# Kernel optimization log

Measured on AMD Instinct MI355X. Metric: run time of the kernel, lower is better.

Reference implementation:

```python
import jax, jax.numpy as jnp
import numpy as np

N_NODES = 50000


def _degrees(idx, n):
    d = jax.ops.segment_sum(jnp.ones(idx.shape, jnp.float32), idx, num_segments=n)
    return jnp.clip(d, 1.0)  # DGL clamps degree at 1


def gcn_layer(x, src, dst, W, b, n):
    """DGL GraphConv with norm='both': D_dst^-1/2 * sum_edges(D_src^-1/2 * x_src) @ W + b.
    Applies W before aggregation when in_feats > out_feats (cheaper), matching DGL."""
    inv_sqrt_out = _degrees(src, n) ** -0.5  # out-degree norm on source side
    inv_sqrt_in = _degrees(dst, n) ** -0.5   # in-degree norm on dest side
    h = x * inv_sqrt_out[:, None]
    if W.shape[0] > W.shape[1]:
        h = h @ W
        agg = jax.ops.segment_sum(h[src], dst, num_segments=n)
    else:
        agg = jax.ops.segment_sum(h[src], dst, num_segments=n)
        agg = agg @ W
    return agg * inv_sqrt_in[:, None] + b


def setup_inputs() -> dict:
    key = jax.random.key(0)
    ks = jax.random.split(key, 8)
    E = 800000
    in_feat = jax.random.normal(ks[0], (N_NODES, 1), dtype=jnp.float32)
    edge_index = jax.random.randint(ks[1], (2, E), 0, N_NODES, dtype=jnp.int32)
    def glorot(k, fan_in, fan_out):
        s = (6.0 / (fan_in + fan_out)) ** 0.5
        return jax.random.uniform(k, (fan_in, fan_out), jnp.float32, -s, s)
    W0 = glorot(ks[2], 1, 100); b0 = jnp.zeros((100,), jnp.float32)
    W1 = glorot(ks[3], 100, 10); b1 = jnp.zeros((10,), jnp.float32)
    W2 = glorot(ks[4], 10, 1); b2 = jnp.zeros((1,), jnp.float32)
    return {"in_feat": in_feat, "edge_index": edge_index,
            "W0": W0, "b0": b0, "W1": W1, "b1": b1, "W2": W2, "b2": b2}


def reference(in_feat, edge_index, W0, b0, W1, b1, W2, b2):
    src, dst = edge_index[0], edge_index[1]
    n = N_NODES
    h = gcn_layer(in_feat, src, dst, W0, b0, n)
    h = jax.nn.leaky_relu(h, negative_slope=0.01)
    h = gcn_layer(h, src, dst, W1, b1, n)
    h = jax.nn.relu(h)
    h = gcn_layer(h, src, dst, W2, b2, n)
    h = jax.nn.relu(h)
    return h
```

## Files before the change

### kernel.cpp

```cpp
#include <hip/hip_runtime.h>


#define NT 256
#define NTB 1024
#define K_BKT 250
#define R_NODES 200
#define SEG 48
#define CAP 4096
#define CHUNK 4096
#define BIN_BLOCKS 196
#define NSLOT (BIN_BLOCKS * SEG)
#define FINF 3.0e38f


__global__ __launch_bounds__(NT) void k_bin(const int4* __restrict__ src4,
                                            const int4* __restrict__ dst4, int E4,
                                            unsigned short* __restrict__ cntd16,
                                            unsigned short* __restrict__ cnts16,
                                            unsigned* __restrict__ dstSeg,
                                            unsigned short* __restrict__ srcSeg) {
  __shared__ unsigned cnt_d[K_BKT], cnt_s[K_BKT];
  int t = threadIdx.x, blk = blockIdx.x;
  for (int k = t; k < K_BKT; k += NT) { cnt_d[k] = 0u; cnt_s[k] = 0u; }
  __syncthreads();
  int base4 = blk * (CHUNK / 4);
  int4 sA[4], dA[4];
#pragma unroll
  for (int j = 0; j < 4; j++) {
    int e4 = base4 + j * NT + t;
    if (e4 < E4) { sA[j] = src4[e4]; dA[j] = dst4[e4]; }
    else { sA[j] = make_int4(-1, -1, -1, -1); dA[j] = make_int4(-1, -1, -1, -1); }
  }
  const int* sp = (const int*)sA;
  const int* dp = (const int*)dA;
#pragma unroll
  for (int j = 0; j < 16; j++) {
    int d = dp[j], s = sp[j];
    if (d >= 0) {
      unsigned bd = (unsigned)d / R_NODES;
      unsigned pd = atomicAdd(&cnt_d[bd], 1u);
      if (pd < SEG)
        dstSeg[((size_t)bd * BIN_BLOCKS + blk) * SEG + pd] =
            (unsigned)s | (((unsigned)d - bd * R_NODES) << 16);
      unsigned bs = (unsigned)s / R_NODES;
      unsigned ps = atomicAdd(&cnt_s[bs], 1u);
      if (ps < SEG)
        srcSeg[((size_t)bs * BIN_BLOCKS + blk) * SEG + ps] =
            (unsigned short)((unsigned)s - bs * R_NODES);
    }
  }
  __syncthreads();
  for (int k = t; k < K_BKT; k += NT) {
    unsigned cd = cnt_d[k]; if (cd > SEG) cd = SEG;
    unsigned cs = cnt_s[k]; if (cs > SEG) cs = SEG;
    cntd16[(size_t)blk * K_BKT + k] = (unsigned short)cd;
    cnts16[(size_t)blk * K_BKT + k] = (unsigned short)cs;
  }
}


struct BktLds {
  unsigned dslab[NSLOT];
  unsigned short sslab[NSLOT];
  unsigned cnt[R_NODES], cnts[R_NODES], cur[R_NODES];
  unsigned sc[256];
  unsigned short crow_d[256], crow_s[256];
  unsigned short stage[CAP];
};
struct PreLds {
  float W0s[100], b0s[100], W1s[1000];
  float beta[100], bsorted[128];
  int ord[100];
  float cA[1000], cB[1000];
  float baseA[16], baseB[16];
};
union BPool { BktLds b; PreLds p; };

__global__ __launch_bounds__(NTB) void k_bucket(
    const unsigned short* __restrict__ cntd16, const unsigned short* __restrict__ cnts16,
    const unsigned* __restrict__ dstSeg, const unsigned short* __restrict__ srcSeg,
    const float* __restrict__ x,
    const float* __restrict__ W0, const float* __restrict__ b0,
    const float* __restrict__ W1,
    float* __restrict__ betas, float* __restrict__ Aseg, float* __restrict__ Bseg,
    unsigned short* __restrict__ csr16,
    unsigned* __restrict__ rs, unsigned* __restrict__ rd,
    float* __restrict__ dsrc_inv, float* __restrict__ ddst_inv,
    float* __restrict__ s0, int n, int nbin) {
  __shared__ BPool u;
  int t = threadIdx.x, blk = blockIdx.x;
  if (blk < K_BKT) {
    const int b = blk;
    const int4* dsl4 = (const int4*)(dstSeg + (size_t)b * NSLOT);
    int4* dl4 = (int4*)u.b.dslab;
    for (int i = t; i < NSLOT / 4; i += NTB) dl4[i] = dsl4[i];
    const int4* ssl4 = (const int4*)(srcSeg + (size_t)b * NSLOT);
    int4* sl4 = (int4*)u.b.sslab;
    for (int i = t; i < NSLOT / 8; i += NTB) sl4[i] = ssl4[i];
    if (t < 256) {
      u.b.crow_d[t] = (t < nbin) ? cntd16[(size_t)t * K_BKT + b] : (unsigned short)0;
      u.b.crow_s[t] = (t < nbin) ? cnts16[(size_t)t * K_BKT + b] : (unsigned short)0;
    }
    for (int k = t; k < R_NODES; k += NTB) { u.b.cnt[k] = 0u; u.b.cnts[k] = 0u; }
    __syncthreads();
    for (int sl = t; sl < NSLOT; sl += NTB) {
      int blkI = sl / SEG, idx = sl - blkI * SEG;
      if (idx < (int)u.b.crow_d[blkI]) atomicAdd(&u.b.cnt[u.b.dslab[sl] >> 16], 1u);
      if (idx < (int)u.b.crow_s[blkI]) atomicAdd(&u.b.cnts[u.b.sslab[sl]], 1u);
    }
    __syncthreads();
    unsigned v = 0u;
    if (t < 256) {
      v = (t < R_NODES) ? u.b.cnt[t] : 0u;
      u.b.sc[t] = v;
    }
    __syncthreads();
    for (int off = 1; off < 256; off <<= 1) {
      unsigned a = (t >= off && t < 256) ? u.b.sc[t - off] : 0u;
      __syncthreads();
      if (t < 256) u.b.sc[t] += a;
      __syncthreads();
    }
    if (t < R_NODES) {
      unsigned st = u.b.sc[t] - v;
      int vg = b * R_NODES + t;
      if (vg < n) {
        unsigned di = u.b.cnt[t], dou = u.b.cnts[t];
        rs[vg] = (unsigned)b * CAP + st;
        rd[vg] = di;
        ddst_inv[vg] = rsqrtf((float)(di < 1u ? 1u : di));
        float ia = rsqrtf((float)(dou < 1u ? 1u : dou));
        dsrc_inv[vg] = ia;
        s0[vg] = x[vg] * ia;
      }
      u.b.cur[t] = st;
    }
    __syncthreads();
    for (int sl = t; sl < NSLOT; sl += NTB) {
      int blkI = sl / SEG, idx = sl - blkI * SEG;
      if (idx < (int)u.b.crow_d[blkI]) {
        unsigned e = u.b.dslab[sl];
        unsigned pos = atomicAdd(&u.b.cur[e >> 16], 1u);
        if (pos < CAP) u.b.stage[pos] = (unsigned short)(e & 0xFFFFu);
      }
    }
    __syncthreads();
    unsigned nd = u.b.sc[255]; if (nd > CAP) nd = CAP;
    int4* cg4 = (int4*)(csr16 + (size_t)b * CAP);
    const int4* st4 = (const int4*)u.b.stage;
    unsigned nv = (nd + 7) / 8;
    for (unsigned i = t; i < nv; i += NTB) cg4[i] = st4[i];
  } else {
    if (t < 100) { u.p.W0s[t] = W0[t]; u.p.b0s[t] = b0[t]; }
    for (int k = t; k < 1000; k += NTB) u.p.W1s[k] = W1[k];
    __syncthreads();
    if (t < 100) {
      float w = u.p.W0s[t];
      u.p.beta[t] = (w != 0.0f) ? (-u.p.b0s[t] / w) : FINF;
    }
    __syncthreads();
    if (t < 100) {
      float bt = u.p.beta[t];
      int r = 0;
      for (int j = 0; j < 100; j++) {
        float bj = u.p.beta[j];
        r += (bj < bt || (bj == bt && j < t)) ? 1 : 0;
      }
      u.p.bsorted[r] = bt;
      u.p.ord[r] = t;
    }
    if (t >= 100 && t < 128) u.p.bsorted[t] = FINF;
    __syncthreads();
    if (t < 128) betas[t] = u.p.bsorted[t];
    if (t < 1000) {
      int k = t / 10, j = t - k * 10;
      int f = u.p.ord[k];
      float w = u.p.W0s[f];
      float w1 = u.p.W1s[f * 10 + j];
      float ca = 0.0f, cb = 0.0f;
      if (w != 0.0f) {
        ca = 0.99f * fabsf(w) * w1;
        cb = 0.99f * ((w > 0.0f) ? 1.0f : -1.0f) * u.p.b0s[f] * w1;
      }
      u.p.cA[t] = ca;
      u.p.cB[t] = cb;
    }
    if (t < 10) {
      const int j = t;
      float a = 0.0f, bacc = 0.0f;
      for (int f = 0; f < 100; f++) {
        float w = u.p.W0s[f], bb = u.p.b0s[f], w1 = u.p.W1s[f * 10 + j];
        if (w == 0.0f) {
          float h = bb >= 0.0f ? bb : 0.01f * bb;
          bacc += h * w1;
        } else {
          float cc = (w > 0.0f) ? 0.01f : 1.0f;
          a += cc * w * w1;
          bacc += cc * bb * w1;
        }
      }
      Aseg[j] = a; Bseg[j] = bacc;
      u.p.baseA[j] = a; u.p.baseB[j] = bacc;
    }
    __syncthreads();
    for (int off = 1; off < 100; off <<= 1) {
      float a = 0.0f, bv = 0.0f;
      bool act = (t < 1000) && (t / 10 >= off);
      if (act) { a = u.p.cA[t - off * 10]; bv = u.p.cB[t - off * 10]; }
      __syncthreads();
      if (act) { u.p.cA[t] += a; u.p.cB[t] += bv; }
      __syncthreads();
    }
    if (t < 1000) {
      int k = t / 10, j = t - k * 10;
      Aseg[(k + 1) * 10 + j] = u.p.baseA[j] + u.p.cA[t];
      Bseg[(k + 1) * 10 + j] = u.p.baseB[j] + u.p.cB[t];
    }
  }
}


__global__ void k_g_l0l1(const unsigned* __restrict__ rs, const unsigned* __restrict__ rd,
                         const unsigned short* __restrict__ csr16,
                         const float* __restrict__ s0,
                         const float* __restrict__ dsrc_inv, const float* __restrict__ ddst_inv,
                         const float* __restrict__ betas,
                         const float* __restrict__ Aseg, const float* __restrict__ Bseg,
                         float* __restrict__ t1, int n) {
  __shared__ float bs_[128], As[1010], Bs[1010];
  for (int k = threadIdx.x; k < 128; k += blockDim.x) bs_[k] = betas[k];
  for (int k = threadIdx.x; k < 1010; k += blockDim.x) { As[k] = Aseg[k]; Bs[k] = Bseg[k]; }
  __syncthreads();
  int tid = blockIdx.x * blockDim.x + threadIdx.x;
  int v = tid >> 2, k4 = tid & 3;
  if (v >= n) return;
  unsigned base = rs[v], deg = rd[v];
  const unsigned short* row = csr16 + base;
  float c = 0.0f;
#pragma unroll 4
  for (unsigned i = k4; i < deg; i += 4) c += s0[row[i]];
  c += __shfl_xor(c, 1, 4);
  c += __shfl_xor(c, 2, 4);
  float c0 = c * ddst_inv[v];
  int lo = 0, hi = 100;
#pragma unroll
  for (int it = 0; it < 7; it++) {
    int mid = (lo + hi) >> 1;
    bool go = bs_[mid] < c0;
    lo = go ? mid + 1 : lo;
    hi = go ? hi : mid;
  }
  float so = dsrc_inv[v];
  for (int j = k4; j < 10; j += 4)
    t1[v * 10 + j] = fmaf(c0, As[lo * 10 + j], Bs[lo * 10 + j]) * so;
}

__global__ void k_g10_l1l2(const unsigned* __restrict__ rs, const unsigned* __restrict__ rd,
                           const unsigned short* __restrict__ csr16,
                           const float* __restrict__ t1,
                           const float* __restrict__ dsrc_inv, const float* __restrict__ ddst_inv,
                           const float* __restrict__ b1, const float* __restrict__ W2,
                           float* __restrict__ t2, int n) {
  int tid = blockIdx.x * blockDim.x + threadIdx.x;
  int v = tid >> 4, f = tid & 15;
  if (v >= n) return;
  unsigned base = rs[v], deg = rd[v];
  const unsigned short* row = csr16 + base;
  int r0 = row[f], r1 = row[f + 16], r2 = row[f + 32];
  float acc = 0.0f;
  for (unsigned i = 0; i < deg; i++) {
    int sv;
    if (i < 48u) {
      int which = i >> 4;
      int rsel = (which == 0) ? r0 : ((which == 1) ? r1 : r2);
      sv = __shfl(rsel, (int)(i & 15u), 16);
    } else {
      sv = row[i];
    }
    if (f < 10) acc += t1[(unsigned)sv * 10 + f];
  }
  float p = 0.0f;
  if (f < 10) {
    float h = acc * ddst_inv[v] + b1[f];
    h = h > 0.0f ? h : 0.0f;
    p = h * W2[f];
  }
  p += __shfl_xor(p, 1, 16);
  p += __shfl_xor(p, 2, 16);
  p += __shfl_xor(p, 4, 16);
  p += __shfl_xor(p, 8, 16);
  if (f == 0) t2[v] = p * dsrc_inv[v];
}

__global__ void k_g_out(const unsigned* __restrict__ rs, const unsigned* __restrict__ rd,
                        const unsigned short* __restrict__ csr16,
                        const float* __restrict__ t2, const float* __restrict__ ddst_inv,
                        const float* __restrict__ b2, float* __restrict__ out, int n) {
  int tid = blockIdx.x * blockDim.x + threadIdx.x;
  int v = tid >> 2, k4 = tid & 3;
  if (v >= n) return;
  unsigned base = rs[v], deg = rd[v];
  const unsigned short* row = csr16 + base;
  float c = 0.0f;
#pragma unroll 4
  for (unsigned i = k4; i < deg; i += 4) c += t2[row[i]];
  c += __shfl_xor(c, 1, 4);
  c += __shfl_xor(c, 2, 4);
  if (k4 == 0) {
    float h = c * ddst_inv[v] + b2[0];
    out[v] = h > 0.0f ? h : 0.0f;
  }
}

extern "C" void kernel_launch(void* const* d_in, const int* in_sizes, int n_in,
                              void* d_out, int out_size, void* d_ws, size_t ws_size,
                              hipStream_t stream) {
  const float* in_feat = (const float*)d_in[0];
  const int* ei = (const int*)d_in[1];
  const float* W0 = (const float*)d_in[2];
  const float* b0 = (const float*)d_in[3];
  const float* W1 = (const float*)d_in[4];
  const float* b1 = (const float*)d_in[5];
  const float* W2 = (const float*)d_in[6];
  const float* b2 = (const float*)d_in[7];
  float* out = (float*)d_out;

  const int n = in_sizes[0];
  const int E = in_sizes[1] / 2;
  const int* src = ei;
  const int* dst = ei + E;
  const int E4 = E / 4;
  int nbin = (E + CHUNK - 1) / CHUNK;
  if (nbin > BIN_BLOCKS) nbin = BIN_BLOCKS;

  unsigned short* cntd16 = (unsigned short*)d_ws;
  unsigned short* cnts16 = cntd16 + (size_t)BIN_BLOCKS * K_BKT;
  unsigned* dstSeg = (unsigned*)(cnts16 + (size_t)BIN_BLOCKS * K_BKT);
  unsigned short* srcSeg = (unsigned short*)(dstSeg + (size_t)K_BKT * NSLOT);
  unsigned short* csr16 = srcSeg + (size_t)K_BKT * NSLOT;
  unsigned* rs = (unsigned*)(csr16 + (size_t)K_BKT * CAP + 64);
  unsigned* rd = rs + n;
  float* dsrc_inv = (float*)(rd + n);
  float* ddst_inv = dsrc_inv + n;
  float* s0 = ddst_inv + n;
  float* t1 = s0 + n;
  float* t2 = t1 + 10 * n;
  float* betas = t2 + n;
  float* Aseg = betas + 128;
  float* Bseg = Aseg + 1010;

  k_bin<<<nbin, NT, 0, stream>>>((const int4*)src, (const int4*)dst, E4,
                                 cntd16, cnts16, dstSeg, srcSeg);
  k_bucket<<<K_BKT + 1, NTB, 0, stream>>>(cntd16, cnts16, dstSeg, srcSeg, in_feat,
                                          W0, b0, W1, betas, Aseg, Bseg, csr16,
                                          rs, rd, dsrc_inv, ddst_inv, s0, n, nbin);
  k_g_l0l1<<<(4 * n + NT - 1) / NT, NT, 0, stream>>>(rs, rd, csr16, s0, dsrc_inv, ddst_inv,
                                                     betas, Aseg, Bseg, t1, n);
  k_g10_l1l2<<<(16 * n + NT - 1) / NT, NT, 0, stream>>>(rs, rd, csr16, t1, dsrc_inv, ddst_inv,
                                                        b1, W2, t2, n);
  k_g_out<<<(4 * n + NT - 1) / NT, NT, 0, stream>>>(rs, rd, csr16, t2, ddst_inv, b2, out, n);
}
```

Measured before the change: 65.20 us.

## Pass compact per-node segment descriptors instead of 10-wide features to layer-1 gather

Layer 0 now writes a 16-byte float4 per node (scaled value, source norm, segment index) instead of a 10-float feature row. The layer-1 gather loads these descriptors cooperatively and rebuilds each neighbour's 10 features from shared-memory segment tables with two FMAs. This shrinks the random gather traffic per edge. In exchange it adds shuffles and shared-memory reads per neighbour, plus a table load into every block of the 16-thread-per-node kernel.

```diff
diff --git a/kernel.cpp b/kernel.cpp
--- a/kernel.cpp
+++ b/kernel.cpp
@@ -225,11 +225,9 @@
                          const float* __restrict__ s0,
                          const float* __restrict__ dsrc_inv, const float* __restrict__ ddst_inv,
                          const float* __restrict__ betas,
-                         const float* __restrict__ Aseg, const float* __restrict__ Bseg,
-                         float* __restrict__ t1, int n) {
-  __shared__ float bs_[128], As[1010], Bs[1010];
+                         float4* __restrict__ y4, int n) {
+  __shared__ float bs_[128];
   for (int k = threadIdx.x; k < 128; k += blockDim.x) bs_[k] = betas[k];
-  for (int k = threadIdx.x; k < 1010; k += blockDim.x) { As[k] = Aseg[k]; Bs[k] = Bseg[k]; }
   __syncthreads();
   int tid = blockIdx.x * blockDim.x + threadIdx.x;
   int v = tid >> 2, k4 = tid & 3;
@@ -250,34 +248,43 @@
     lo = go ? mid + 1 : lo;
     hi = go ? hi : mid;
   }
-  float so = dsrc_inv[v];
-  for (int j = k4; j < 10; j += 4)
-    t1[v * 10 + j] = fmaf(c0, As[lo * 10 + j], Bs[lo * 10 + j]) * so;
+  if (k4 == 0) {
+    float so = dsrc_inv[v];
+    y4[v] = make_float4(so * c0, so, __int_as_float(lo), 0.0f);
+  }
 }
 
 __global__ void k_g10_l1l2(const unsigned* __restrict__ rs, const unsigned* __restrict__ rd,
                            const unsigned short* __restrict__ csr16,
-                           const float* __restrict__ t1,
+                           const float4* __restrict__ y4,
                            const float* __restrict__ dsrc_inv, const float* __restrict__ ddst_inv,
+                           const float* __restrict__ Aseg, const float* __restrict__ Bseg,
                            const float* __restrict__ b1, const float* __restrict__ W2,
                            float* __restrict__ t2, int n) {
+  __shared__ float As[1010], Bs[1010];
+  for (int k = threadIdx.x; k < 1010; k += blockDim.x) { As[k] = Aseg[k]; Bs[k] = Bseg[k]; }
+  __syncthreads();
   int tid = blockIdx.x * blockDim.x + threadIdx.x;
   int v = tid >> 4, f = tid & 15;
   if (v >= n) return;
   unsigned base = rs[v], deg = rd[v];
   const unsigned short* row = csr16 + base;
-  int r0 = row[f], r1 = row[f + 16], r2 = row[f + 32];
   float acc = 0.0f;
-  for (unsigned i = 0; i < deg; i++) {
-    int sv;
-    if (i < 48u) {
-      int which = i >> 4;
-      int rsel = (which == 0) ? r0 : ((which == 1) ? r1 : r2);
-      sv = __shfl(rsel, (int)(i & 15u), 16);
-    } else {
-      sv = row[i];
-    }
-    if (f < 10) acc += t1[(unsigned)sv * 10 + f];
+  for (unsigned c = 0; c < deg; c += 16u) {
+    unsigned i = c + (unsigned)f;
+    int idx = (i < deg) ? (int)row[i] : 0;
+    float4 y = y4[idx];
+    unsigned m = deg - c; if (m > 16u) m = 16u;
+    for (unsigned j = 0; j < m; j++) {
+      float soc = __shfl(y.x, (int)j, 16);
+      float so = __shfl(y.y, (int)j, 16);
+      int sg = __shfl(__float_as_int(y.z), (int)j, 16);
+      if (f < 10) {
+        int o = sg * 10 + f;
+        acc = fmaf(soc, As[o], acc);
+        acc = fmaf(so, Bs[o], acc);
+      }
+    }
   }
   float p = 0.0f;
   if (f < 10) {
@@ -343,8 +350,8 @@
   float* dsrc_inv = (float*)(rd + n);
   float* ddst_inv = dsrc_inv + n;
   float* s0 = ddst_inv + n;
-  float* t1 = s0 + n;
-  float* t2 = t1 + 10 * n;
+  float4* y4 = (float4*)(s0 + n);
+  float* t2 = (float*)(y4 + n);
   float* betas = t2 + n;
   float* Aseg = betas + 128;
   float* Bseg = Aseg + 1010;
@@ -355,8 +362,8 @@
                                           W0, b0, W1, betas, Aseg, Bseg, csr16,
                                           rs, rd, dsrc_inv, ddst_inv, s0, n, nbin);
   k_g_l0l1<<<(4 * n + NT - 1) / NT, NT, 0, stream>>>(rs, rd, csr16, s0, dsrc_inv, ddst_inv,
-                                                     betas, Aseg, Bseg, t1, n);
-  k_g10_l1l2<<<(16 * n + NT - 1) / NT, NT, 0, stream>>>(rs, rd, csr16, t1, dsrc_inv, ddst_inv,
-                                                        b1, W2, t2, n);
+                                                     betas, y4, n);
+  k_g10_l1l2<<<(16 * n + NT - 1) / NT, NT, 0, stream>>>(rs, rd, csr16, y4, dsrc_inv, ddst_inv,
+                                                        Aseg, Bseg, b1, W2, t2, n);
   k_g_out<<<(4 * n + NT - 1) / NT, NT, 0, stream>>>(rs, rd, csr16, t2, ddst_inv, b2, out, n);
 }
```

Measured after the change: 61.36 us (median of 2 runs). 5.9% less time.
